# Kernel optimization log

Hardware: AMD Instinct MI355X
Metric: run time of the kernel (lower is better)

The kernel has to match this reference:

```python
import math
import jax, jax.numpy as jnp
import numpy as np

B, S, D, H = 2, 4096, 512, 8
DH = D // H


def setup_inputs() -> dict:
    key = jax.random.key(0)
    ks = jax.random.split(key, 12)
    lim = 1.0 / math.sqrt(D)
    u = lambda k, shp: jax.random.uniform(k, shp, jnp.float32, -lim, lim)
    return {
        "x": jax.random.normal(ks[0], (B, S, D), jnp.float32),
        "gamma": jax.random.uniform(ks[1], (B, S, 1), jnp.float32),
        "Wq": u(ks[2], (D, D)), "bq": u(ks[3], (D,)),
        "Wk": u(ks[4], (D, D)), "bk": u(ks[5], (D,)),
        "Wv": u(ks[6], (D, D)), "bv": u(ks[7], (D,)),
        "Wo": u(ks[8], (D, D)), "bo": u(ks[9], (D,)),
    }


def reference(x, gamma, Wq, bq, Wk, bk, Wv, bv, Wo, bo):
    b, s, d = x.shape
    # projections (torch Linear: x @ W.T + b), split heads -> [B,H,S,DH]
    def proj(W, bias):
        return (x @ W.T + bias).reshape(b, s, H, DH).transpose(0, 2, 1, 3)
    q, k, v = proj(Wq, bq), proj(Wk, bk), proj(Wv, bv)

    scores = jnp.einsum("bhsd,bhtd->bhst", q, k) / math.sqrt(DH)  # [B,H,S,S]
    causal = jnp.triu(jnp.ones((s, s), bool), k=1)  # True above diagonal
    neg_inf = jnp.float32(-jnp.inf)
    scores = jnp.where(causal[None, None], neg_inf, scores)

    # hyperbolic positional bias: -log1p(gamma_i * max(i-j, 0) + 1e-8)
    pos = jnp.arange(s)
    delta = jnp.clip(pos[:, None] - pos[None, :], 0).astype(jnp.float32)  # [S,S]
    gamma_q = gamma[:, :, 0][:, :, None]  # [B,S,1]
    hyper = -jnp.log1p(gamma_q * delta + 1e-8)  # [B,S,S]
    hyper = jnp.where(causal[None], neg_inf, hyper)
    scores = scores + hyper[:, None]  # [B,H,S,S]

    attn = jax.nn.softmax(scores, axis=-1)
    out = jnp.einsum("bhst,bhtd->bhsd", attn, v)  # [B,H,S,DH]
    out = out.transpose(0, 2, 1, 3).reshape(b, s, d)
    return out @ Wo.T + bo
```

## Files before the change

kernel.cpp:

```cpp
#include <hip/hip_runtime.h>
#include <hip/hip_bf16.h>

#define Bb 2
#define Ss 4096
#define Dd 512
#define Hh 8
#define DHh 64

typedef __attribute__((ext_vector_type(8))) short short8;
typedef __attribute__((ext_vector_type(4))) float floatx4;

static __device__ __forceinline__ ushort bfbits(float f) {
  union { __hip_bfloat16 h; ushort u; } cv;
  cv.h = __float2bfloat16(f);
  return cv.u;
}

static __device__ __forceinline__ unsigned int packhi(float a, float b) {
  union { float f; unsigned int u; } ca, cb; ca.f = a; cb.f = b;
  return (ca.u >> 16) | (cb.u & 0xffff0000u);
}

__global__ void cvt_all(const float* __restrict__ x,
                        const float* __restrict__ w0, const float* __restrict__ w1,
                        const float* __restrict__ w2, const float* __restrict__ w3,
                        ushort* __restrict__ out) {
  const int XN4 = (Bb * Ss * Dd) / 4;
  const int WN4 = (Dd * Dd) / 4;
  int i = blockIdx.x * blockDim.x + threadIdx.x;
  if (i >= XN4 + 4 * WN4) return;
  const float* s; int li;
  if (i < XN4) { s = x; li = i; }
  else {
    int t = i - XN4; int j = t >> 16; li = t & (WN4 - 1);
    s = (j == 0) ? w0 : (j == 1) ? w1 : (j == 2) ? w2 : w3;
  }
  float4 f = ((const float4*)s)[li];
  ushort4 u;
  u.x = bfbits(f.x); u.y = bfbits(f.y); u.z = bfbits(f.z); u.w = bfbits(f.w);
  ((ushort4*)out)[i] = u;
}

static __device__ __forceinline__ int vperm(int s0) {
  int kb = (s0 >> 4) & 3, gq = (s0 >> 2) & 3;
  return (s0 & ~63) | ((kb >> 1) << 5) | (gq << 3) | ((kb & 1) << 2);
}

#define LDQK(buf, k0)                                                          \
  _Pragma("unroll")                                                            \
  for (int rb = 0; rb < 4; ++rb)                                               \
    af[buf][rb] = *(const short8*)(ap + (size_t)rb * 16 * 512 + (k0));         \
  _Pragma("unroll")                                                            \
  for (int cb = 0; cb < 4; ++cb)                                               \
    bf[buf][cb] = *(const short8*)(bp + (size_t)cb * 16 * 512 + (k0));

__global__ __launch_bounds__(256) void qkv_gemm(
    const ushort* __restrict__ xb,
    const ushort* __restrict__ Wq, const ushort* __restrict__ Wk, const ushort* __restrict__ Wv,
    const float* __restrict__ bq, const float* __restrict__ bk, const float* __restrict__ bv,
    ushort* __restrict__ qo, ushort* __restrict__ ko, ushort* __restrict__ vo)
{
  int mb = blockIdx.x / 12, rest = blockIdx.x % 12;
  int which = rest >> 2, nb = rest & 3;
  const ushort* Bw  = (which == 0) ? Wq : (which == 1) ? Wk : Wv;
  const float* bias = (which == 0) ? bq : (which == 1) ? bk : bv;
  int lane = threadIdx.x & 63, w = threadIdx.x >> 6;
  int wr = w & 1, wc = w >> 1;
  int g = lane >> 4, ln = lane & 15;
  int m0 = mb * 128 + wr * 64;
  int c0 = nb * 128 + wc * 64;
  const ushort* ap = xb + (size_t)(m0 + ln) * 512 + g * 8;
  const ushort* bp = Bw + (size_t)(c0 + ln) * 512 + g * 8;
  floatx4 acc[4][4] = {};
  short8 af[2][4], bf[2][4];
  LDQK(0, 0)
#pragma unroll
  for (int it = 0; it < 16; ++it) {
    int cur = it & 1;
    if (it < 15) { LDQK(cur ^ 1, (it + 1) * 32) }
#pragma unroll
    for (int rb = 0; rb < 4; ++rb)
#pragma unroll
      for (int cb = 0; cb < 4; ++cb)
        acc[rb][cb] = __builtin_amdgcn_mfma_f32_16x16x32_bf16(af[cur][rb], bf[cur][cb], acc[rb][cb], 0, 0, 0);
  }
  float scale = (which == 0) ? 0.125f * 1.44269504f : 1.0f;
#pragma unroll
  for (int rb = 0; rb < 4; ++rb)
#pragma unroll
    for (int cb = 0; cb < 4; ++cb) {
      int col = c0 + cb * 16 + ln;
      float bv_ = bias[col];
      int hh = col >> 6, dh = col & 63;
      if (which == 2) {
        int i0 = m0 + rb * 16 + g * 4;
        int bI = i0 >> 12, s0 = i0 & (Ss - 1);
        ushort4 pk;
        pk.x = bfbits(acc[rb][cb][0] + bv_);
        pk.y = bfbits(acc[rb][cb][1] + bv_);
        pk.z = bfbits(acc[rb][cb][2] + bv_);
        pk.w = bfbits(acc[rb][cb][3] + bv_);
        *(ushort4*)(vo + (((size_t)bI * Hh + hh) * DHh + dh) * Ss + vperm(s0)) = pk;
      } else {
        ushort* outp = (which == 0) ? qo : ko;
#pragma unroll
        for (int r = 0; r < 4; ++r) {
          int i = m0 + rb * 16 + g * 4 + r;
          int bI = i >> 12, s = i & (Ss - 1);
          outp[(((size_t)bI * Hh + hh) * Ss + s) * DHh + dh] = bfbits((acc[rb][cb][r] + bv_) * scale);
        }
      }
    }
}

#define LD32(buf, k0)                                                          \
  af[buf][0] = *(const short8*)(ap + (k0));                                    \
  af[buf][1] = *(const short8*)(ap + 16 * 512 + (k0));                         \
  _Pragma("unroll")                                                            \
  for (int ns = 0; ns < 4; ++ns)                                               \
    bfr[buf][ns] = *(const short8*)(bp + (size_t)ns * 16 * 512 + (k0));

__global__ __launch_bounds__(256) void gemm_out(
    const ushort* __restrict__ A, const ushort* __restrict__ Bw,
    const float* __restrict__ bias, float* __restrict__ outp)
{
  int mb = blockIdx.x >> 3, nb = blockIdx.x & 7;
  int lane = threadIdx.x & 63, w = threadIdx.x >> 6;
  int g = lane >> 4, ln = lane & 15;
  int m0 = mb * 128 + w * 32;
  const ushort* ap = A + (size_t)(m0 + ln) * 512 + g * 8;
  const ushort* bp = Bw + (size_t)(nb * 64 + ln) * 512 + g * 8;
  floatx4 acc[2][4] = {};
  short8 af[2][2], bfr[2][4];
  LD32(0, 0)
#pragma unroll
  for (int it = 0; it < 16; ++it) {
    int cur = it & 1;
    if (it < 15) { LD32(cur ^ 1, (it + 1) * 32) }
#pragma unroll
    for (int ns = 0; ns < 4; ++ns) {
      acc[0][ns] = __builtin_amdgcn_mfma_f32_16x16x32_bf16(af[cur][0], bfr[cur][ns], acc[0][ns], 0, 0, 0);
      acc[1][ns] = __builtin_amdgcn_mfma_f32_16x16x32_bf16(af[cur][1], bfr[cur][ns], acc[1][ns], 0, 0, 0);
    }
  }
#pragma unroll
  for (int rb = 0; rb < 2; ++rb)
#pragma unroll
    for (int ns = 0; ns < 4; ++ns) {
      int col = nb * 64 + ns * 16 + ln;
      float bv_ = bias[col];
#pragma unroll
      for (int r = 0; r < 4; ++r)
        outp[(size_t)(m0 + rb * 16 + g * 4 + r) * 512 + col] = acc[rb][ns][r] + bv_;
    }
}

__global__ __launch_bounds__(192) void flash8(
    const ushort* __restrict__ q, const ushort* __restrict__ k,
    const ushort* __restrict__ vt, const float* __restrict__ gamma,
    ushort* __restrict__ o)
{
  __shared__ __align__(16) float Pmrg[2][64][34];
  __shared__ __align__(16) ushort Tb[16 * 72];

  int z = blockIdx.x;
  int bh = z & 15, tq = z >> 4;
  int b = bh >> 3, hh = bh & 7;
  int tid = threadIdx.x;
  int wv = tid >> 6, lane = tid & 63;
  int g = lane >> 4, ln = lane & 15;

  const ushort* kp = k + ((size_t)bh * Ss + ln) * DHh + g * 8;
  const ushort* vp = vt + ((size_t)bh * DHh + ln) * Ss + g * 8;

#pragma unroll 1
  for (int rep = 0; rep < 2; ++rep) {
    int t = rep ? (127 - tq) : tq;
    int q0 = t * 32;
    int nkt = (t >> 1) + 1;
    int ktm = nkt - 1;
    int lo = (nkt * wv) / 3, hi = (nkt * (wv + 1)) / 3;

    const ushort* qp = q + ((size_t)bh * Ss + q0 + ln) * DHh + g * 8;
    short8 qf00 = *(const short8*)qp;
    short8 qf01 = *(const short8*)(qp + 32);
    short8 qf10 = *(const short8*)(qp + 16 * DHh);
    short8 qf11 = *(const short8*)(qp + 16 * DHh + 32);

    int qrow0 = q0 + ln, qrow1 = q0 + 16 + ln;
    float gm0 = gamma[(size_t)b * Ss + qrow0];
    float gm1 = gamma[(size_t)b * Ss + qrow1];
    float l2[2] = {0.0f, 0.0f};
    floatx4 oacc[2][4] = {};

    short8 kfl[4], kfh[4], vf[8];
    int kb0 = lo * 64;
#pragma unroll
    for (int ns = 0; ns < 4; ++ns) {
      kfl[ns] = *(const short8*)(kp + (size_t)(kb0 + ns * 16) * DHh);
      kfh[ns] = *(const short8*)(kp + (size_t)(kb0 + ns * 16) * DHh + 32);
    }
#pragma unroll
    for (int cc = 0; cc < 8; ++cc)
      vf[cc] = *(const short8*)(vp + (size_t)((cc & 3) * 16) * Ss + kb0 + (cc >> 2) * 32);

    for (int kt = lo; kt < hi; ++kt) {
      int kbase = kt * 64;
      float sv[2][16];
#pragma unroll
      for (int ns = 0; ns < 4; ++ns) {
        floatx4 z0 = {}, z1 = {};
        z0 = __builtin_amdgcn_mfma_f32_16x16x32_bf16(kfl[ns], qf00, z0, 0, 0, 0);
        z0 = __builtin_amdgcn_mfma_f32_16x16x32_bf16(kfh[ns], qf01, z0, 0, 0, 0);
        z1 = __builtin_amdgcn_mfma_f32_16x16x32_bf16(kfl[ns], qf10, z1, 0, 0, 0);
        z1 = __builtin_amdgcn_mfma_f32_16x16x32_bf16(kfh[ns], qf11, z1, 0, 0, 0);
#pragma unroll
        for (int r = 0; r < 4; ++r) { sv[0][ns * 4 + r] = z0[r]; sv[1][ns * 4 + r] = z1[r]; }
      }
      if (kt + 1 < hi) {
        const ushort* kn = kp + (size_t)(kbase + 64) * DHh;
#pragma unroll
        for (int ns = 0; ns < 4; ++ns) {
          kfl[ns] = *(const short8*)(kn + (size_t)(ns * 16) * DHh);
          kfh[ns] = *(const short8*)(kn + (size_t)(ns * 16) * DHh + 32);
        }
      }
      bool last = (kt == ktm);
      short8 pfrag[2][2];
#pragma unroll
      for (int qb = 0; qb < 2; ++qb) {
        int qrow = qb ? qrow1 : qrow0;
        float gm = qb ? gm1 : gm0;
        int db = qrow - kbase - g * 4;
        float fd = (float)db;
        float rs = 0.0f;
        if (last) {
#pragma unroll
          for (int e = 0; e < 16; ++e)
            if (db - (e >> 2) * 16 - (e & 3) < 0) sv[qb][e] = -1e30f;
#pragma unroll
          for (int e = 0; e < 16; ++e) {
            float delta = fmaxf(fd - (float)((e >> 2) * 16 + (e & 3)), 0.0f);
            float wt = __builtin_amdgcn_rcpf(fmaf(gm, delta, 1.0f));
            float pv = __builtin_amdgcn_exp2f(sv[qb][e]) * wt;
            rs += pv;
            sv[qb][e] = pv;
          }
        } else {
#pragma unroll
          for (int e = 0; e < 16; ++e) {
            float delta = fd - (float)((e >> 2) * 16 + (e & 3));
            float wt = __builtin_amdgcn_rcpf(fmaf(gm, delta, 1.0f));
            float pv = __builtin_amdgcn_exp2f(sv[qb][e]) * wt;
            rs += pv;
            sv[qb][e] = pv;
          }
        }
        l2[qb] += rs;
#pragma unroll
        for (int c = 0; c < 2; ++c) {
          uint4 pkd;
          pkd.x = packhi(sv[qb][8 * c + 0], sv[qb][8 * c + 1]);
          pkd.y = packhi(sv[qb][8 * c + 2], sv[qb][8 * c + 3]);
          pkd.z = packhi(sv[qb][8 * c + 4], sv[qb][8 * c + 5]);
          pkd.w = packhi(sv[qb][8 * c + 6], sv[qb][8 * c + 7]);
          pfrag[qb][c] = *(short8*)&pkd;
        }
      }
#pragma unroll
      for (int c = 0; c < 2; ++c)
#pragma unroll
        for (int ds = 0; ds < 4; ++ds) {
          oacc[0][ds] = __builtin_amdgcn_mfma_f32_16x16x32_bf16(vf[c * 4 + ds], pfrag[0][c], oacc[0][ds], 0, 0, 0);
          oacc[1][ds] = __builtin_amdgcn_mfma_f32_16x16x32_bf16(vf[c * 4 + ds], pfrag[1][c], oacc[1][ds], 0, 0, 0);
        }
      if (kt + 1 < hi) {
#pragma unroll
        for (int cc = 0; cc < 8; ++cc)
          vf[cc] = *(const short8*)(vp + (size_t)((cc & 3) * 16) * Ss + kbase + 64 + (cc >> 2) * 32);
      }
    }

    __syncthreads();
    if (wv) {
#pragma unroll
      for (int qb = 0; qb < 2; ++qb)
#pragma unroll
        for (int ds = 0; ds < 4; ++ds)
#pragma unroll
          for (int r = 0; r < 4; ++r)
            Pmrg[wv - 1][lane][qb * 16 + ds * 4 + r] = oacc[qb][ds][r];
      Pmrg[wv - 1][lane][32] = l2[0];
      Pmrg[wv - 1][lane][33] = l2[1];
    }
    __syncthreads();
    if (!wv) {
#pragma unroll
      for (int qb = 0; qb < 2; ++qb) {
        float l = l2[qb];
#pragma unroll
        for (int w2 = 0; w2 < 2; ++w2) {
#pragma unroll
          for (int ds = 0; ds < 4; ++ds)
#pragma unroll
            for (int r = 0; r < 4; ++r)
              oacc[qb][ds][r] += Pmrg[w2][lane][qb * 16 + ds * 4 + r];
          l += Pmrg[w2][lane][32 + qb];
        }
        l += __shfl_xor(l, 16);
        l += __shfl_xor(l, 32);
        float linv = 1.0f / l;
#pragma unroll
        for (int ds = 0; ds < 4; ++ds)
#pragma unroll
          for (int r = 0; r < 4; ++r)
            Tb[ln * 72 + ds * 16 + g * 4 + r] = bfbits(oacc[qb][ds][r] * linv);
        short8 v0 = *(const short8*)(Tb + ln * 72 + g * 16);
        short8 v1 = *(const short8*)(Tb + ln * 72 + g * 16 + 8);
        size_t oa = ((size_t)b * Ss + q0 + qb * 16 + ln) * Dd + hh * DHh + g * 16;
        *(short8*)(o + oa) = v0;
        *(short8*)(o + oa + 8) = v1;
      }
    }
  }
}

extern "C" void kernel_launch(void* const* d_in, const int* in_sizes, int n_in,
                              void* d_out, int out_size, void* d_ws, size_t ws_size,
                              hipStream_t stream) {
  const float* x     = (const float*)d_in[0];
  const float* gamma = (const float*)d_in[1];
  const float* Wq    = (const float*)d_in[2];
  const float* bq    = (const float*)d_in[3];
  const float* Wk    = (const float*)d_in[4];
  const float* bk    = (const float*)d_in[5];
  const float* Wv    = (const float*)d_in[6];
  const float* bv    = (const float*)d_in[7];
  const float* Wo    = (const float*)d_in[8];
  const float* bo    = (const float*)d_in[9];

  const size_t NX = (size_t)Bb * Ss * Dd;
  const size_t NW = (size_t)Dd * Dd;
  ushort* xb  = (ushort*)d_ws;
  ushort* Wqb = xb + NX;
  ushort* Wkb = Wqb + NW;
  ushort* Wvb = Wkb + NW;
  ushort* Wob = Wvb + NW;
  ushort* qb  = Wob + NW;
  ushort* kb  = qb + NX;
  ushort* vtb = kb + NX;
  ushort* ab  = vtb + NX;

  const int total4 = (int)(NX / 4 + 4 * (NW / 4));
  cvt_all<<<(total4 + 255) / 256, 256, 0, stream>>>(x, Wq, Wk, Wv, Wo, xb);

  qkv_gemm<<<64 * 12, 256, 0, stream>>>(xb, Wqb, Wkb, Wvb, bq, bk, bv, qb, kb, vtb);

  flash8<<<1024, 192, 0, stream>>>(qb, kb, vtb, gamma, ab);

  gemm_out<<<512, 256, 0, stream>>>(ab, Wob, bo, (float*)d_out);
}
```

Baseline: 298.8 us.

## Split flash attention by query rows per wave instead of splitting keys

Each of four waves in a block now owns its own 32-row query tile inside a 128-row group, iterating over all causal key tiles, instead of three waves splitting one query tile's key range. This removes the shared-memory partial merge and the two block barriers, so each wave normalizes and writes its own output. It also remaps block indices to interleave batch/head and pairs query groups for load balance. In exchange, waves within a block carry unequal work (a diagonal skew), and K/V loads are no longer shared across the split.

```diff
diff --git a/kernel.cpp b/kernel.cpp
--- a/kernel.cpp
+++ b/kernel.cpp
@@ -155,16 +155,16 @@
     }
 }
 
-__global__ __launch_bounds__(192) void flash8(
+__global__ __launch_bounds__(256) void flash10(
     const ushort* __restrict__ q, const ushort* __restrict__ k,
     const ushort* __restrict__ vt, const float* __restrict__ gamma,
     ushort* __restrict__ o)
 {
-  __shared__ __align__(16) float Pmrg[2][64][34];
-  __shared__ __align__(16) ushort Tb[16 * 72];
+  __shared__ __align__(16) ushort Tb[4][16 * 72];
 
   int z = blockIdx.x;
-  int bh = z & 15, tq = z >> 4;
+  int bh = ((z & 7) << 1) | ((z >> 3) & 1);
+  int p = z >> 4;
   int b = bh >> 3, hh = bh & 7;
   int tid = threadIdx.x;
   int wv = tid >> 6, lane = tid & 63;
@@ -175,11 +175,10 @@
 
 #pragma unroll 1
   for (int rep = 0; rep < 2; ++rep) {
-    int t = rep ? (127 - tq) : tq;
-    int q0 = t * 32;
-    int nkt = (t >> 1) + 1;
-    int ktm = nkt - 1;
-    int lo = (nkt * wv) / 3, hi = (nkt * (wv + 1)) / 3;
+    int gq = rep ? (31 - p) : p;
+    int q0 = gq * 128 + wv * 32;
+    int hi = 2 * gq + (wv >> 1) + 1;
+    int ktm = hi - 1;
 
     const ushort* qp = q + ((size_t)bh * Ss + q0 + ln) * DHh + g * 8;
     short8 qf00 = *(const short8*)qp;
@@ -194,18 +193,18 @@
     floatx4 oacc[2][4] = {};
 
     short8 kfl[4], kfh[4], vf[8];
-    int kb0 = lo * 64;
 #pragma unroll
     for (int ns = 0; ns < 4; ++ns) {
-      kfl[ns] = *(const short8*)(kp + (size_t)(kb0 + ns * 16) * DHh);
-      kfh[ns] = *(const short8*)(kp + (size_t)(kb0 + ns * 16) * DHh + 32);
+      kfl[ns] = *(const short8*)(kp + (size_t)(ns * 16) * DHh);
+      kfh[ns] = *(const short8*)(kp + (size_t)(ns * 16) * DHh + 32);
     }
 #pragma unroll
     for (int cc = 0; cc < 8; ++cc)
-      vf[cc] = *(const short8*)(vp + (size_t)((cc & 3) * 16) * Ss + kb0 + (cc >> 2) * 32);
-
-    for (int kt = lo; kt < hi; ++kt) {
+      vf[cc] = *(const short8*)(vp + (size_t)((cc & 3) * 16) * Ss + (cc >> 2) * 32);
+
+    for (int kt = 0; kt < hi; ++kt) {
       int kbase = kt * 64;
+      bool more = (kt + 1 < hi);
       float sv[2][16];
 #pragma unroll
       for (int ns = 0; ns < 4; ++ns) {
@@ -217,7 +216,7 @@
 #pragma unroll
         for (int r = 0; r < 4; ++r) { sv[0][ns * 4 + r] = z0[r]; sv[1][ns * 4 + r] = z1[r]; }
       }
-      if (kt + 1 < hi) {
+      if (more) {
         const ushort* kn = kp + (size_t)(kbase + 64) * DHh;
 #pragma unroll
         for (int ns = 0; ns < 4; ++ns) {
@@ -274,53 +273,30 @@
           oacc[0][ds] = __builtin_amdgcn_mfma_f32_16x16x32_bf16(vf[c * 4 + ds], pfrag[0][c], oacc[0][ds], 0, 0, 0);
           oacc[1][ds] = __builtin_amdgcn_mfma_f32_16x16x32_bf16(vf[c * 4 + ds], pfrag[1][c], oacc[1][ds], 0, 0, 0);
         }
-      if (kt + 1 < hi) {
+      if (more) {
 #pragma unroll
         for (int cc = 0; cc < 8; ++cc)
           vf[cc] = *(const short8*)(vp + (size_t)((cc & 3) * 16) * Ss + kbase + 64 + (cc >> 2) * 32);
       }
     }
 
-    __syncthreads();
-    if (wv) {
-#pragma unroll
-      for (int qb = 0; qb < 2; ++qb)
-#pragma unroll
-        for (int ds = 0; ds < 4; ++ds)
-#pragma unroll
-          for (int r = 0; r < 4; ++r)
-            Pmrg[wv - 1][lane][qb * 16 + ds * 4 + r] = oacc[qb][ds][r];
-      Pmrg[wv - 1][lane][32] = l2[0];
-      Pmrg[wv - 1][lane][33] = l2[1];
-    }
-    __syncthreads();
-    if (!wv) {
-#pragma unroll
-      for (int qb = 0; qb < 2; ++qb) {
-        float l = l2[qb];
-#pragma unroll
-        for (int w2 = 0; w2 < 2; ++w2) {
-#pragma unroll
-          for (int ds = 0; ds < 4; ++ds)
-#pragma unroll
-            for (int r = 0; r < 4; ++r)
-              oacc[qb][ds][r] += Pmrg[w2][lane][qb * 16 + ds * 4 + r];
-          l += Pmrg[w2][lane][32 + qb];
-        }
-        l += __shfl_xor(l, 16);
-        l += __shfl_xor(l, 32);
-        float linv = 1.0f / l;
-#pragma unroll
-        for (int ds = 0; ds < 4; ++ds)
-#pragma unroll
-          for (int r = 0; r < 4; ++r)
-            Tb[ln * 72 + ds * 16 + g * 4 + r] = bfbits(oacc[qb][ds][r] * linv);
-        short8 v0 = *(const short8*)(Tb + ln * 72 + g * 16);
-        short8 v1 = *(const short8*)(Tb + ln * 72 + g * 16 + 8);
-        size_t oa = ((size_t)b * Ss + q0 + qb * 16 + ln) * Dd + hh * DHh + g * 16;
-        *(short8*)(o + oa) = v0;
-        *(short8*)(o + oa + 8) = v1;
-      }
+    ushort* tb = &Tb[wv][0];
+#pragma unroll
+    for (int qb = 0; qb < 2; ++qb) {
+      float l = l2[qb];
+      l += __shfl_xor(l, 16);
+      l += __shfl_xor(l, 32);
+      float linv = 1.0f / l;
+#pragma unroll
+      for (int ds = 0; ds < 4; ++ds)
+#pragma unroll
+        for (int r = 0; r < 4; ++r)
+          tb[ln * 72 + ds * 16 + g * 4 + r] = bfbits(oacc[qb][ds][r] * linv);
+      short8 v0 = *(const short8*)(tb + ln * 72 + g * 16);
+      short8 v1 = *(const short8*)(tb + ln * 72 + g * 16 + 8);
+      size_t oa = ((size_t)b * Ss + q0 + qb * 16 + ln) * Dd + hh * DHh + g * 16;
+      *(short8*)(o + oa) = v0;
+      *(short8*)(o + oa + 8) = v1;
     }
   }
 }
@@ -356,7 +332,7 @@
 
   qkv_gemm<<<64 * 12, 256, 0, stream>>>(xb, Wqb, Wkb, Wvb, bq, bk, bv, qb, kb, vtb);
 
-  flash8<<<1024, 192, 0, stream>>>(qb, kb, vtb, gamma, ab);
+  flash10<<<512, 256, 0, stream>>>(qb, kb, vtb, gamma, ab);
 
   gemm_out<<<512, 256, 0, stream>>>(ab, Wob, bo, (float*)d_out);
 }
```

Result: slower. 400.0 us (+33.9%).
